# Performance work log

Measured on AMD Instinct MI355X. Metric: run time of the kernel, lower is better.

## Reference

```python
import jax, jax.numpy as jnp
import numpy as np

MODEL_DIM = 1024
NUM_HEADS = 16
HEAD_DIM = MODEL_DIM // NUM_HEADS


def setup_inputs() -> dict:
    key = jax.random.key(0)
    ks = jax.random.split(key, 9)
    s = 1.0 / np.sqrt(MODEL_DIM)
    d = {
        "query": jax.random.normal(ks[0], (2, 2048, MODEL_DIM), dtype=jnp.float32),
        "Wq": jax.random.normal(ks[1], (MODEL_DIM, MODEL_DIM), dtype=jnp.float32) * s,
        "bq": jnp.zeros((MODEL_DIM,), dtype=jnp.float32),
        "Wk": jax.random.normal(ks[2], (MODEL_DIM, MODEL_DIM), dtype=jnp.float32) * s,
        "bk": jnp.zeros((MODEL_DIM,), dtype=jnp.float32),
        "Wv": jax.random.normal(ks[3], (MODEL_DIM, MODEL_DIM), dtype=jnp.float32) * s,
        "bv": jnp.zeros((MODEL_DIM,), dtype=jnp.float32),
        "Wo": jax.random.normal(ks[4], (MODEL_DIM, MODEL_DIM), dtype=jnp.float32) * s,
        "bo": jnp.zeros((MODEL_DIM,), dtype=jnp.float32),
    }
    return d


def reference(query, Wq, bq, Wk, bk, Wv, bv, Wo, bo):
    B, S, D = query.shape
    H, hd = NUM_HEADS, HEAD_DIM
    # self-attention: key = value = query
    q = (query @ Wq.T + bq).reshape(B, S, H, hd).transpose(0, 2, 1, 3)  # [B,H,S,hd]
    k = (query @ Wk.T + bk).reshape(B, S, H, hd).transpose(0, 2, 1, 3)
    v = (query @ Wv.T + bv).reshape(B, S, H, hd).transpose(0, 2, 1, 3)
    scores = jnp.einsum("bhqd,bhkd->bhqk", q, k) / np.sqrt(hd)  # [B,H,S,S]
    attn = jax.nn.softmax(scores, axis=-1)
    ctx = jnp.einsum("bhqk,bhkd->bhqd", attn, v)  # [B,H,S,hd]
    ctx = ctx.transpose(0, 2, 1, 3).reshape(B, S, D)
    return ctx @ Wo.T + bo
```

## Files before the change

### kernel.cpp

```cpp
#include <hip/hip_runtime.h>

typedef __attribute__((ext_vector_type(8))) __bf16 bf16x8;
typedef __attribute__((ext_vector_type(8))) unsigned short ushort8;
typedef __attribute__((ext_vector_type(4))) unsigned short ushort4v;
typedef __attribute__((ext_vector_type(4))) float f32x4;
typedef __attribute__((ext_vector_type(4))) _Float16 f16x4;
typedef __attribute__((ext_vector_type(8))) _Float16 f16x8;

__device__ __forceinline__ unsigned short f2bf(float f) {
    union { float f; unsigned int u; } c; c.f = f;
    unsigned int u = c.u;
    u += 0x7fffu + ((u >> 16) & 1u);
    return (unsigned short)(u >> 16);
}

__device__ __forceinline__ void async16(const void* g, void* l) {
    __builtin_amdgcn_global_load_lds(
        (const __attribute__((address_space(1))) unsigned int*)g,
        (__attribute__((address_space(3))) unsigned int*)l, 16, 0, 0);
}

__global__ __launch_bounds__(256) void cvt_f32_bf16(const float* __restrict__ src,
                                                    unsigned short* __restrict__ dst, int n,
                                                    float scale) {
    int i = (blockIdx.x * 256 + threadIdx.x) * 4;
    if (i >= n) return;
    float4 v = *(const float4*)(src + i);
    ushort4v o;
    o[0] = f2bf(v.x * scale); o[1] = f2bf(v.y * scale);
    o[2] = f2bf(v.z * scale); o[3] = f2bf(v.w * scale);
    *(ushort4v*)(dst + i) = o;
}

template<int OUT_BF16>
__global__ __launch_bounds__(256) void gemm_bt(
    const unsigned short* __restrict__ A,
    const unsigned short* __restrict__ B,
    void* __restrict__ Cout,
    const float* __restrict__ b0, const float* __restrict__ b1, const float* __restrict__ b2,
    float s0, float s1, float s2,
    int M, int N, int K)
{
    __shared__ __align__(16) unsigned short As[128 * 32];
    __shared__ __align__(16) unsigned short Bs[128 * 32];

    const int tid  = threadIdx.x;
    const int lane = tid & 63, wave = tid >> 6;
    const int quad = lane >> 4, l15 = lane & 15;
    const int wm = wave >> 1, wn = wave & 1;
    const int by = blockIdx.y, bx = blockIdx.x;

    const int srow = lane >> 2;
    const int sp   = lane & 3;
    const int scl  = sp ^ ((srow >> 1) & 3);
    const int swz  = (l15 >> 1) & 3;

    f32x4 acc[4][4];
#pragma unroll
    for (int i = 0; i < 4; ++i)
#pragma unroll
        for (int j = 0; j < 4; ++j) acc[i][j] = (f32x4)(0.0f);

    const int nk = K >> 5;
    for (int kt = 0; kt < nk; ++kt) {
        __syncthreads();
#pragma unroll
        for (int i = 0; i < 2; ++i) {
            int row = i * 64 + wave * 16 + srow;
            async16(A + (size_t)(by * 128 + row) * K + kt * 32 + scl * 8,
                    &As[(i * 64 + wave * 16) * 32]);
            async16(B + (size_t)(bx * 128 + row) * K + kt * 32 + scl * 8,
                    &Bs[(i * 64 + wave * 16) * 32]);
        }
        __syncthreads();

        bf16x8 af[4], bfr[4];
#pragma unroll
        for (int mi = 0; mi < 4; ++mi)
            af[mi] = __builtin_bit_cast(bf16x8,
                *(const ushort8*)&As[(wm * 64 + mi * 16 + l15) * 32 + (quad ^ swz) * 8]);
#pragma unroll
        for (int ni = 0; ni < 4; ++ni)
            bfr[ni] = __builtin_bit_cast(bf16x8,
                *(const ushort8*)&Bs[(wn * 64 + ni * 16 + l15) * 32 + (quad ^ swz) * 8]);
#pragma unroll
        for (int mi = 0; mi < 4; ++mi)
#pragma unroll
            for (int ni = 0; ni < 4; ++ni)
                acc[mi][ni] = __builtin_amdgcn_mfma_f32_16x16x32_bf16(af[mi], bfr[ni], acc[mi][ni], 0, 0, 0);
    }

#pragma unroll
    for (int ni = 0; ni < 4; ++ni) {
        int n = bx * 128 + wn * 64 + ni * 16 + l15;
        float bias = (n < 1024) ? b0[n] * s0 : (n < 2048 ? b1[n - 1024] * s1 : b2[n - 2048] * s2);
#pragma unroll
        for (int mi = 0; mi < 4; ++mi) {
#pragma unroll
            for (int r = 0; r < 4; ++r) {
                int m = by * 128 + wm * 64 + mi * 16 + quad * 4 + r;
                float v = acc[mi][ni][r] + bias;
                if (OUT_BF16) ((unsigned short*)Cout)[(size_t)m * N + n] = f2bf(v);
                else          ((float*)Cout)[(size_t)m * N + n] = v;
            }
        }
    }
}

__global__ __launch_bounds__(256) void transpose_v(const unsigned short* __restrict__ qkv,
                                                   _Float16* __restrict__ vtg)
{
    __shared__ unsigned short Ls[64][68];
    const int tid = threadIdx.x;
    const int bh = blockIdx.y, st = blockIdx.x;
    const int b = bh >> 4, h = bh & 15;

#pragma unroll
    for (int i = 0; i < 2; ++i) {
        int s = tid + i * 256;
        int row = s >> 3, c8 = (s & 7) << 3;
        ushort8 v = *(const ushort8*)(qkv + (size_t)(b * 2048 + st * 64 + row) * 3072 + 2048 + h * 64 + c8);
        *(ushort8*)&Ls[row][c8] = v;
    }
    __syncthreads();
#pragma unroll
    for (int i = 0; i < 2; ++i) {
        int s = tid + i * 256;
        int hd = s >> 3, p = s & 7;
        int cl = p ^ (hd & 7);
        int g = cl >> 2, q = cl & 3;
        f16x8 o;
#pragma unroll
        for (int e = 0; e < 8; ++e) {
            int kv = g * 32 + (e >> 2) * 16 + q * 4 + (e & 3);
            union { float f; unsigned int u; } c;
            c.u = ((unsigned int)Ls[kv][hd]) << 16;
            o[e] = (_Float16)c.f;
        }
        *(f16x8*)(vtg + (size_t)(bh * 64 + hd) * 2048 + st * 64 + p * 8) = o;
    }
}

__global__ __launch_bounds__(256) void attn(const unsigned short* __restrict__ qkv,
                                            const _Float16* __restrict__ vtg,
                                            unsigned short* __restrict__ ctx)
{
    __shared__ __align__(16) unsigned short Ks[64 * 64];
    __shared__ __align__(16) _Float16 Vt[64 * 64];

    const int tid  = threadIdx.x;
    const int lane = tid & 63, wave = tid >> 6;
    const int quad = lane >> 4, l15 = lane & 15;
    const int bh = blockIdx.y;
    const int b = bh >> 4, h = bh & 15;
    const int q0 = blockIdx.x * 64;
    const int qrow = b * 2048 + q0 + wave * 16 + l15;

    const int srow = lane >> 3;
    const int sp   = lane & 7;
    const int scl  = sp ^ srow;
    const int sw   = l15 & 7;

    bf16x8 qf[2];
#pragma unroll
    for (int kh = 0; kh < 2; ++kh)
        qf[kh] = __builtin_bit_cast(bf16x8,
            *(const ushort8*)(qkv + (size_t)qrow * 3072 + h * 64 + kh * 32 + quad * 8));

    f32x4 ot[4];
#pragma unroll
    for (int ht = 0; ht < 4; ++ht) ot[ht] = (f32x4)(0.0f);
    float l_acc = 0.0f;

    for (int kt = 0; kt < 32; ++kt) {
        __syncthreads();
#pragma unroll
        for (int i = 0; i < 2; ++i) {
            int row = i * 32 + wave * 8 + srow;
            async16(qkv + (size_t)(b * 2048 + kt * 64 + row) * 3072 + 1024 + h * 64 + scl * 8,
                    &Ks[(i * 32 + wave * 8) * 64]);
            async16(vtg + (size_t)(bh * 64 + row) * 2048 + kt * 64 + sp * 8,
                    (unsigned short*)&Vt[(i * 32 + wave * 8) * 64]);
        }
        __syncthreads();

        f16x4 pv[4];
#pragma unroll
        for (int mt = 0; mt < 4; ++mt) {
            const unsigned short* kb = &Ks[(mt * 16 + l15) * 64];
            bf16x8 k0 = __builtin_bit_cast(bf16x8, *(const ushort8*)(kb + (quad ^ sw) * 8));
            bf16x8 k1 = __builtin_bit_cast(bf16x8, *(const ushort8*)(kb + ((quad ^ sw) ^ 4) * 8));
            f32x4 s4 = (f32x4)(0.0f);
            s4 = __builtin_amdgcn_mfma_f32_16x16x32_bf16(k0, qf[0], s4, 0, 0, 0);
            s4 = __builtin_amdgcn_mfma_f32_16x16x32_bf16(k1, qf[1], s4, 0, 0, 0);
#pragma unroll
            for (int r = 0; r < 4; ++r) {
                float p = __builtin_amdgcn_exp2f(s4[r]);
                l_acc += p;
                pv[mt][r] = (_Float16)p;
            }
        }

#pragma unroll
        for (int ht = 0; ht < 4; ++ht) {
            const _Float16* vb = &Vt[(ht * 16 + l15) * 64];
#pragma unroll
            for (int g = 0; g < 2; ++g) {
                f16x8 v8 = *(const f16x8*)(vb + (((g * 4 + quad) ^ sw)) * 8);
                f16x4 vlo = __builtin_shufflevector(v8, v8, 0, 1, 2, 3);
                f16x4 vhi = __builtin_shufflevector(v8, v8, 4, 5, 6, 7);
                ot[ht] = __builtin_amdgcn_mfma_f32_16x16x16f16(vlo, pv[2 * g],     ot[ht], 0, 0, 0);
                ot[ht] = __builtin_amdgcn_mfma_f32_16x16x16f16(vhi, pv[2 * g + 1], ot[ht], 0, 0, 0);
            }
        }
    }

    l_acc += __shfl_xor(l_acc, 16, 64);
    l_acc += __shfl_xor(l_acc, 32, 64);
    float inv = 1.0f / l_acc;

#pragma unroll
    for (int ht = 0; ht < 4; ++ht) {
        ushort4v o4;
#pragma unroll
        for (int r = 0; r < 4; ++r) o4[r] = f2bf(ot[ht][r] * inv);
        *(ushort4v*)(ctx + (size_t)qrow * 1024 + h * 64 + ht * 16 + quad * 4) = o4;
    }
}

extern "C" void kernel_launch(void* const* d_in, const int* in_sizes, int n_in,
                              void* d_out, int out_size, void* d_ws, size_t ws_size,
                              hipStream_t stream) {
    const float* query = (const float*)d_in[0];
    const float* Wq = (const float*)d_in[1];
    const float* bq = (const float*)d_in[2];
    const float* Wk = (const float*)d_in[3];
    const float* bk = (const float*)d_in[4];
    const float* Wv = (const float*)d_in[5];
    const float* bv = (const float*)d_in[6];
    const float* Wo = (const float*)d_in[7];
    const float* bo = (const float*)d_in[8];

    char* ws = (char*)d_ws;
    unsigned short* q_bf  = (unsigned short*)(ws);
    _Float16*       vtg   = (_Float16*)(ws);
    unsigned short* wqkv  = (unsigned short*)(ws + 8388608);
    unsigned short* wo_bf = (unsigned short*)(ws + 14680064);
    unsigned short* qkv   = (unsigned short*)(ws + 16777216);
    unsigned short* ctx   = (unsigned short*)(ws + 41943040);

    const float SCALE = 0.125f * 1.4426950408889634f;
    const int NQ = 4096 * 1024, NW = 1024 * 1024;
    cvt_f32_bf16<<<(NQ / 4 + 255) / 256, 256, 0, stream>>>(query, q_bf, NQ, 1.0f);
    cvt_f32_bf16<<<(NW / 4 + 255) / 256, 256, 0, stream>>>(Wq, wqkv, NW, 1.0f);
    cvt_f32_bf16<<<(NW / 4 + 255) / 256, 256, 0, stream>>>(Wk, wqkv + NW, NW, SCALE);
    cvt_f32_bf16<<<(NW / 4 + 255) / 256, 256, 0, stream>>>(Wv, wqkv + 2 * NW, NW, 1.0f);
    cvt_f32_bf16<<<(NW / 4 + 255) / 256, 256, 0, stream>>>(Wo, wo_bf, NW, 1.0f);

    gemm_bt<1><<<dim3(24, 32), 256, 0, stream>>>(q_bf, wqkv, qkv, bq, bk, bv,
                                                 1.0f, SCALE, 1.0f, 4096, 3072, 1024);
    transpose_v<<<dim3(32, 32), 256, 0, stream>>>(qkv, vtg);
    attn<<<dim3(32, 32), 256, 0, stream>>>(qkv, vtg, ctx);
    gemm_bt<0><<<dim3(8, 32), 256, 0, stream>>>(ctx, wo_bf, d_out, bo, bo, bo,
                                                1.0f, 1.0f, 1.0f, 4096, 1024, 1024);
}
```

Measured before the change: 219.8 us.

## Fuse conversion kernels, widen GEMM K-tile, split-K output projection with atomics

Merges the five f32-to-bf16 conversion launches into one kernel that dispatches on index range. Doubles the GEMM K-tile from 32 to 64, using a new XOR swizzle, so each barrier pair covers twice the MFMA work. Splits the output projection GEMM's K dimension across two blocks along z. The partial sums are accumulated with float atomics into an output zeroed by a memset, raising the block count from 256 to 512 to fill more CUs. This adds a memset, atomic traffic and non-deterministic summation order, and doubles the LDS used per block.

```diff
diff --git a/kernel.cpp b/kernel.cpp
--- a/kernel.cpp
+++ b/kernel.cpp
@@ -20,40 +20,51 @@
         (__attribute__((address_space(3))) unsigned int*)l, 16, 0, 0);
 }
 
-__global__ __launch_bounds__(256) void cvt_f32_bf16(const float* __restrict__ src,
-                                                    unsigned short* __restrict__ dst, int n,
-                                                    float scale) {
+__global__ __launch_bounds__(256) void cvt_all(
+    const float* __restrict__ q,  const float* __restrict__ wq,
+    const float* __restrict__ wk, const float* __restrict__ wv,
+    const float* __restrict__ wo,
+    unsigned short* __restrict__ q_bf, unsigned short* __restrict__ wqkv,
+    unsigned short* __restrict__ wo_bf, float scale_k)
+{
+    const int NQ = 4096 * 1024, NW = 1024 * 1024;
     int i = (blockIdx.x * 256 + threadIdx.x) * 4;
-    if (i >= n) return;
-    float4 v = *(const float4*)(src + i);
+    const float* src; unsigned short* dst; float sc = 1.0f; int off;
+    if (i < NQ)               { src = q;  dst = q_bf;          off = i; }
+    else if (i < NQ + NW)     { src = wq; dst = wqkv;          off = i - NQ; }
+    else if (i < NQ + 2 * NW) { src = wk; dst = wqkv + NW;     off = i - NQ - NW; sc = scale_k; }
+    else if (i < NQ + 3 * NW) { src = wv; dst = wqkv + 2 * NW; off = i - NQ - 2 * NW; }
+    else                      { src = wo; dst = wo_bf;         off = i - NQ - 3 * NW; }
+    float4 v = *(const float4*)(src + off);
     ushort4v o;
-    o[0] = f2bf(v.x * scale); o[1] = f2bf(v.y * scale);
-    o[2] = f2bf(v.z * scale); o[3] = f2bf(v.w * scale);
-    *(ushort4v*)(dst + i) = o;
-}
-
-template<int OUT_BF16>
+    o[0] = f2bf(v.x * sc); o[1] = f2bf(v.y * sc);
+    o[2] = f2bf(v.z * sc); o[3] = f2bf(v.w * sc);
+    *(ushort4v*)(dst + off) = o;
+}
+
+template<int MODE>
 __global__ __launch_bounds__(256) void gemm_bt(
     const unsigned short* __restrict__ A,
     const unsigned short* __restrict__ B,
     void* __restrict__ Cout,
     const float* __restrict__ b0, const float* __restrict__ b1, const float* __restrict__ b2,
     float s0, float s1, float s2,
-    int M, int N, int K)
-{
-    __shared__ __align__(16) unsigned short As[128 * 32];
-    __shared__ __align__(16) unsigned short Bs[128 * 32];
+    int N, int K, int ksz)
+{
+    __shared__ __align__(16) unsigned short As[128 * 64];
+    __shared__ __align__(16) unsigned short Bs[128 * 64];
 
     const int tid  = threadIdx.x;
     const int lane = tid & 63, wave = tid >> 6;
     const int quad = lane >> 4, l15 = lane & 15;
     const int wm = wave >> 1, wn = wave & 1;
     const int by = blockIdx.y, bx = blockIdx.x;
-
-    const int srow = lane >> 2;
-    const int sp   = lane & 3;
-    const int scl  = sp ^ ((srow >> 1) & 3);
-    const int swz  = (l15 >> 1) & 3;
+    const int k0 = blockIdx.z * ksz;
+
+    const int srow = lane >> 3;
+    const int sp   = lane & 7;
+    const int scl  = sp ^ srow;
+    const int sw   = l15 & 7;
 
     f32x4 acc[4][4];
 #pragma unroll
@@ -61,47 +72,49 @@
 #pragma unroll
         for (int j = 0; j < 4; ++j) acc[i][j] = (f32x4)(0.0f);
 
-    const int nk = K >> 5;
+    const int nk = ksz >> 6;
     for (int kt = 0; kt < nk; ++kt) {
         __syncthreads();
 #pragma unroll
-        for (int i = 0; i < 2; ++i) {
-            int row = i * 64 + wave * 16 + srow;
-            async16(A + (size_t)(by * 128 + row) * K + kt * 32 + scl * 8,
-                    &As[(i * 64 + wave * 16) * 32]);
-            async16(B + (size_t)(bx * 128 + row) * K + kt * 32 + scl * 8,
-                    &Bs[(i * 64 + wave * 16) * 32]);
-        }
-        __syncthreads();
-
-        bf16x8 af[4], bfr[4];
-#pragma unroll
-        for (int mi = 0; mi < 4; ++mi)
-            af[mi] = __builtin_bit_cast(bf16x8,
-                *(const ushort8*)&As[(wm * 64 + mi * 16 + l15) * 32 + (quad ^ swz) * 8]);
-#pragma unroll
-        for (int ni = 0; ni < 4; ++ni)
-            bfr[ni] = __builtin_bit_cast(bf16x8,
-                *(const ushort8*)&Bs[(wn * 64 + ni * 16 + l15) * 32 + (quad ^ swz) * 8]);
-#pragma unroll
-        for (int mi = 0; mi < 4; ++mi)
+        for (int j = 0; j < 4; ++j) {
+            int r0 = wave * 32 + j * 8;
+            async16(A + (size_t)(by * 128 + r0 + srow) * K + k0 + kt * 64 + scl * 8, &As[r0 * 64]);
+            async16(B + (size_t)(bx * 128 + r0 + srow) * K + k0 + kt * 64 + scl * 8, &Bs[r0 * 64]);
+        }
+        __syncthreads();
+
+#pragma unroll
+        for (int kh = 0; kh < 2; ++kh) {
+            bf16x8 af[4], bfr[4];
+#pragma unroll
+            for (int mi = 0; mi < 4; ++mi)
+                af[mi] = __builtin_bit_cast(bf16x8,
+                    *(const ushort8*)&As[(wm * 64 + mi * 16 + l15) * 64 + ((kh * 4 + quad) ^ sw) * 8]);
 #pragma unroll
             for (int ni = 0; ni < 4; ++ni)
-                acc[mi][ni] = __builtin_amdgcn_mfma_f32_16x16x32_bf16(af[mi], bfr[ni], acc[mi][ni], 0, 0, 0);
+                bfr[ni] = __builtin_bit_cast(bf16x8,
+                    *(const ushort8*)&Bs[(wn * 64 + ni * 16 + l15) * 64 + ((kh * 4 + quad) ^ sw) * 8]);
+#pragma unroll
+            for (int mi = 0; mi < 4; ++mi)
+#pragma unroll
+                for (int ni = 0; ni < 4; ++ni)
+                    acc[mi][ni] = __builtin_amdgcn_mfma_f32_16x16x32_bf16(af[mi], bfr[ni], acc[mi][ni], 0, 0, 0);
+        }
     }
 
 #pragma unroll
     for (int ni = 0; ni < 4; ++ni) {
         int n = bx * 128 + wn * 64 + ni * 16 + l15;
         float bias = (n < 1024) ? b0[n] * s0 : (n < 2048 ? b1[n - 1024] * s1 : b2[n - 2048] * s2);
+        if (MODE == 0 && blockIdx.z != 0) bias = 0.0f;
 #pragma unroll
         for (int mi = 0; mi < 4; ++mi) {
 #pragma unroll
             for (int r = 0; r < 4; ++r) {
                 int m = by * 128 + wm * 64 + mi * 16 + quad * 4 + r;
                 float v = acc[mi][ni][r] + bias;
-                if (OUT_BF16) ((unsigned short*)Cout)[(size_t)m * N + n] = f2bf(v);
-                else          ((float*)Cout)[(size_t)m * N + n] = v;
+                if (MODE == 1) ((unsigned short*)Cout)[(size_t)m * N + n] = f2bf(v);
+                else           unsafeAtomicAdd(&((float*)Cout)[(size_t)m * N + n], v);
             }
         }
     }
@@ -250,17 +263,14 @@
     unsigned short* ctx   = (unsigned short*)(ws + 41943040);
 
     const float SCALE = 0.125f * 1.4426950408889634f;
-    const int NQ = 4096 * 1024, NW = 1024 * 1024;
-    cvt_f32_bf16<<<(NQ / 4 + 255) / 256, 256, 0, stream>>>(query, q_bf, NQ, 1.0f);
-    cvt_f32_bf16<<<(NW / 4 + 255) / 256, 256, 0, stream>>>(Wq, wqkv, NW, 1.0f);
-    cvt_f32_bf16<<<(NW / 4 + 255) / 256, 256, 0, stream>>>(Wk, wqkv + NW, NW, SCALE);
-    cvt_f32_bf16<<<(NW / 4 + 255) / 256, 256, 0, stream>>>(Wv, wqkv + 2 * NW, NW, 1.0f);
-    cvt_f32_bf16<<<(NW / 4 + 255) / 256, 256, 0, stream>>>(Wo, wo_bf, NW, 1.0f);
+
+    hipMemsetAsync(d_out, 0, (size_t)out_size * sizeof(float), stream);
+    cvt_all<<<8192, 256, 0, stream>>>(query, Wq, Wk, Wv, Wo, q_bf, wqkv, wo_bf, SCALE);
 
     gemm_bt<1><<<dim3(24, 32), 256, 0, stream>>>(q_bf, wqkv, qkv, bq, bk, bv,
-                                                 1.0f, SCALE, 1.0f, 4096, 3072, 1024);
+                                                 1.0f, SCALE, 1.0f, 3072, 1024, 1024);
     transpose_v<<<dim3(32, 32), 256, 0, stream>>>(qkv, vtg);
     attn<<<dim3(32, 32), 256, 0, stream>>>(qkv, vtg, ctx);
-    gemm_bt<0><<<dim3(8, 32), 256, 0, stream>>>(ctx, wo_bf, d_out, bo, bo, bo,
-                                                1.0f, 1.0f, 1.0f, 4096, 1024, 1024);
-}
+    gemm_bt<0><<<dim3(8, 32, 2), 256, 0, stream>>>(ctx, wo_bf, d_out, bo, bo, bo,
+                                                   1.0f, 1.0f, 1.0f, 1024, 1024, 512);
+}
```

Result: no change. 222.3 us (+1.2%).
